# Optimization experiments

Hardware: AMD Instinct MI355X
Metric: run time of the kernel (lower is better)

## Reference

```python
import jax, jax.numpy as jnp
import numpy as np

B, D, E, K, C = 16384, 256, 16, 4, 10
EPS = 1e-5  # torch LayerNorm default eps


def setup_inputs() -> dict:
    key = jax.random.key(0)
    ks = jax.random.split(key, 5)
    s = 0.02
    return {
        "features": jax.random.normal(ks[0], (B, D), dtype=jnp.float32),
        "router_w": jax.random.normal(ks[1], (D, E), dtype=jnp.float32) * s,
        "router_b": jnp.zeros((E,), dtype=jnp.float32),
        "ln_g": jnp.ones((E, D), dtype=jnp.float32),
        "ln_b": jnp.zeros((E, D), dtype=jnp.float32),
        "w1": jax.random.normal(ks[2], (E, D, D), dtype=jnp.float32) * s,
        "b1": jnp.zeros((E, D), dtype=jnp.float32),
        "w2": jax.random.normal(ks[3], (E, D, C), dtype=jnp.float32) * s,
        "b2": jnp.zeros((E, C), dtype=jnp.float32),
    }


def reference(features, router_w, router_b, ln_g, ln_b, w1, b1, w2, b2):
    # Router: [B,D] @ [D,E] -> [B,E]
    gate_logits = features @ router_w + router_b
    gate_probs = jax.nn.softmax(gate_logits, axis=-1)
    topk_vals, topk_idx = jax.lax.top_k(gate_probs, K)  # [B,K]
    topk_vals = topk_vals / topk_vals.sum(axis=-1, keepdims=True)

    # Shared LayerNorm statistics (per-sample), per-expert affine.
    mu = features.mean(axis=-1, keepdims=True)
    var = ((features - mu) ** 2).mean(axis=-1, keepdims=True)
    xhat = (features - mu) * jax.lax.rsqrt(var + EPS)  # [B,D]
    xn = ln_g[:, None, :] * xhat[None, :, :] + ln_b[:, None, :]  # [E,B,D]

    # All experts densely (batched GEMMs), exact (erf) GELU like torch.
    h = jax.nn.gelu(jnp.einsum('ebd,edh->ebh', xn, w1) + b1[:, None, :],
                    approximate=False)  # [E,B,D]
    all_logits_e = jnp.einsum('ebh,ehc->ebc', h, w2) + b2[:, None, :]  # [E,B,C]
    all_logits = jnp.transpose(all_logits_e, (1, 0, 2))  # [B,E,C]

    # Gather top-k experts' logits and mix their softmaxed probs.
    idx = jnp.broadcast_to(topk_idx[:, :, None], (features.shape[0], K, C))
    selected = jnp.take_along_axis(all_logits, idx, axis=1)  # [B,K,C]
    market_probs = (topk_vals[:, :, None] * jax.nn.softmax(selected, axis=-1)).sum(axis=1)

    all_probs = jax.nn.softmax(all_logits_e, axis=-1)  # [E,B,C]
    return market_probs, all_probs, gate_probs
```

## Files before the change

kernel.cpp:

```cpp
#include <hip/hip_runtime.h>
#include <hip/hip_bf16.h>
#include <stdint.h>


typedef __bf16 bf16;
typedef __bf16 bf16x8 __attribute__((ext_vector_type(8)));
typedef __bf16 bf16x4 __attribute__((ext_vector_type(4)));
typedef float  f32x4  __attribute__((ext_vector_type(4)));

#define XK_OFF   0UL
#define W1T_OFF  8388608UL
#define W2T_OFF  10485760UL
#define B1P_OFF  10616832UL
#define TKI_OFF  10633216UL
#define TKW_OFF  10895360UL

#define APROBS_OFF 163840UL
#define GATE_OFF   2785280UL

#define LOG2E 1.4426950408889634f

__device__ __forceinline__ void gl_lds16(const void* g, void* l) {
  __builtin_amdgcn_global_load_lds((const __attribute__((address_space(1))) void*)g,
                                   (__attribute__((address_space(3))) void*)l, 16, 0, 0);
}

__device__ __forceinline__ uint32_t cvt_pk_bf16(float a, float b) {
  uint32_t r;
  asm("v_cvt_pk_bf16_f32 %0, %1, %2" : "=v"(r) : "v"(a), "v"(b));
  return r;
}

__device__ __forceinline__ float gelu_f(float x) {
  float e = __builtin_amdgcn_exp2f(-2.45541f * x);
  return x * __builtin_amdgcn_rcpf(e + 1.0f);
}

__global__ __launch_bounds__(256) void k_pre(const float* __restrict__ feat,
                                             const float* __restrict__ rw,
                                             const float* __restrict__ rb,
                                             const float* __restrict__ ln_g,
                                             const float* __restrict__ ln_b,
                                             const float* __restrict__ b1,
                                             const float* __restrict__ w1,
                                             const float* __restrict__ w2,
                                             float* __restrict__ out,
                                             char* __restrict__ ws) {
  __shared__ __align__(16) char sm[20736];
  const int bid = blockIdx.x;
  const int t = threadIdx.x;

  if (bid < 256) {
    float (*tile)[68] = (float(*)[68])sm;
    const int e = bid >> 4, kt = (bid >> 2) & 3, nt = bid & 3;
    {
      const int r = t >> 2, cs = t & 3;
      const float* src = w1 + ((size_t)e * 256 + kt * 64 + r) * 256 + nt * 64 + cs * 16;
#pragma unroll
      for (int j = 0; j < 4; ++j) {
        float4 v = *(const float4*)(src + j * 4);
        *(float4*)(&tile[r][cs * 16 + j * 4]) = v;
      }
    }
    __syncthreads();
    {
      const int rn = t >> 2, ks = t & 3;
      const int n = nt * 64 + rn;
      bf16* base = (bf16*)(ws + W1T_OFF) + (size_t)e * 65536;
      float pb = 0.f;
#pragma unroll
      for (int j = 0; j < 4; ++j) {
        int kc = ks * 16 + j * 4;
        int k0 = kt * 64 + kc;
        float4 g4 = *(const float4*)(ln_g + e * 256 + k0);
        float4 l4 = *(const float4*)(ln_b + e * 256 + k0);
        float t0 = tile[kc + 0][rn], t1 = tile[kc + 1][rn];
        float t2 = tile[kc + 2][rn], t3 = tile[kc + 3][rn];
        bf16x4 o;
        o[0] = (bf16)(t0 * g4.x);
        o[1] = (bf16)(t1 * g4.y);
        o[2] = (bf16)(t2 * g4.z);
        o[3] = (bf16)(t3 * g4.w);
        pb += l4.x * t0 + l4.y * t1 + l4.z * t2 + l4.w * t3;
        *(bf16x4*)(base + (k0 >> 5) * 8192 + n * 32 + (k0 & 31)) = o;
      }
      pb += __shfl_xor(pb, 1);
      pb += __shfl_xor(pb, 2);
      if (ks == 0) {
        if (kt == 0) pb += b1[e * 256 + n];
        atomicAdd((float*)(ws + B1P_OFF) + e * 256 + n, pb);
      }
    }
  } else if (bid < 272) {
    const int e = bid - 256;
    const int c = t >> 4, hs = t & 15;
    bf16* dst = (bf16*)(ws + W2T_OFF) + (size_t)e * 4096 + c * 256 + hs * 16;
#pragma unroll
    for (int j4 = 0; j4 < 4; ++j4) {
      bf16x4 o;
#pragma unroll
      for (int j = 0; j < 4; ++j) {
        int h = hs * 16 + j4 * 4 + j;
        float v = (c < 10) ? w2[((size_t)e * 256 + h) * 10 + c] : 0.0f;
        o[j] = (bf16)v;
      }
      *(bf16x4*)(dst + j4 * 4) = o;
    }
  } else {
    float (*rwt)[260] = (float(*)[260])sm;
    float (*xrow)[256] = (float(*)[256])(sm + 16640);
    const int w = t >> 6, l = t & 63;
    const int b = (bid - 272) * 4 + w;

    float4 x4 = *(const float4*)(feat + (size_t)b * 256 + l * 4);

#pragma unroll
    for (int i = 0; i < 16; ++i) {
      int idx = t + 256 * i;
      rwt[idx & 15][idx >> 4] = rw[idx];
    }
    *(float4*)(&xrow[w][l * 4]) = x4;

    float s = x4.x + x4.y + x4.z + x4.w;
    float s2 = x4.x * x4.x + x4.y * x4.y + x4.z * x4.z + x4.w * x4.w;
#pragma unroll
    for (int off = 1; off < 64; off <<= 1) {
      s += __shfl_xor(s, off);
      s2 += __shfl_xor(s2, off);
    }
    float mu = s * (1.0f / 256.0f);
    float var = s2 * (1.0f / 256.0f) - mu * mu;
    float rstd = __builtin_amdgcn_rsqf(var + 1e-5f);
    bf16x4 hb;
    hb[0] = (bf16)((x4.x - mu) * rstd);
    hb[1] = (bf16)((x4.y - mu) * rstd);
    hb[2] = (bf16)((x4.z - mu) * rstd);
    hb[3] = (bf16)((x4.w - mu) * rstd);
    *(bf16x4*)((bf16*)(ws + XK_OFF) + ((size_t)(b >> 7) * 32768) + (l >> 3) * 4096 +
               (b & 127) * 32 + (l & 7) * 4) = hb;

    __syncthreads();

    const int e = l & 15, q = l >> 4;
    float g = 0.f;
#pragma unroll
    for (int i = 0; i < 16; ++i) {
      float4 xv = *(const float4*)(&xrow[w][q * 64 + i * 4]);
      float4 wv = *(const float4*)(&rwt[e][q * 64 + i * 4]);
      g += xv.x * wv.x + xv.y * wv.y + xv.z * wv.z + xv.w * wv.w;
    }
    g += __shfl_xor(g, 16);
    g += __shfl_xor(g, 32);
    g += rb[e];

    float m = g;
#pragma unroll
    for (int off = 1; off < 16; off <<= 1) m = fmaxf(m, __shfl_xor(m, off));
    float p = __builtin_amdgcn_exp2f((g - m) * LOG2E);
    float sum = p;
#pragma unroll
    for (int off = 1; off < 16; off <<= 1) sum += __shfl_xor(sum, off);
    float prob = p * __builtin_amdgcn_rcpf(sum);
    if (q == 0) out[GATE_OFF + (size_t)b * 16 + e] = prob;

    float pv[16];
#pragma unroll
    for (int i = 0; i < 16; ++i) pv[i] = __shfl(prob, i);
    int idxk[4];
    float valk[4];
#pragma unroll
    for (int k = 0; k < 4; ++k) {
      float best = pv[0];
      int bi = 0;
#pragma unroll
      for (int i = 1; i < 16; ++i) {
        if (pv[i] > best) { best = pv[i]; bi = i; }
      }
      valk[k] = best;
      idxk[k] = bi;
#pragma unroll
      for (int i = 0; i < 16; ++i) pv[i] = (i == bi) ? -1.0f : pv[i];
    }
    float wsum = valk[0] + valk[1] + valk[2] + valk[3];
    float rn = __builtin_amdgcn_rcpf(wsum);
    if (l == 0) {
      int4 iv = {idxk[0], idxk[1], idxk[2], idxk[3]};
      float4 wv = {valk[0] * rn, valk[1] * rn, valk[2] * rn, valk[3] * rn};
      *(int4*)(ws + TKI_OFF + (size_t)b * 16) = iv;
      *(float4*)(ws + TKW_OFF + (size_t)b * 16) = wv;
    }
  }
}

__global__ __launch_bounds__(512, 4) void k_moe(const char* __restrict__ ws,
                                                const float* __restrict__ b2g,
                                                float* __restrict__ out) {
  __shared__ __align__(16) char smem[49152];
  const int lin = blockIdx.x;
  const int e = (lin >> 3) & 15;
  const int mt = (lin & 7) * 16 + (lin >> 7);
  const int m0 = mt * 128;
  const int t = threadIdx.x;
  const int wid = t >> 6, l = t & 63;
  const int lq = l >> 4, lr = l & 15;
  const int wnb = wid >> 1;
  const int wsb = wid & 1;

  const uint16_t* xk = (const uint16_t*)(ws + XK_OFF) + (size_t)mt * 32768;
  const uint16_t* w1km = (const uint16_t*)(ws + W1T_OFF) + (size_t)e * 65536;
  const uint16_t* w2t = (const uint16_t*)(ws + W2T_OFF) + (size_t)e * 4096;
  const float* b1p = (const float*)(ws + B1P_OFF) + e * 256;

  const int pn = t >> 3, hf = (t >> 2) & 1, sl = t & 3;
  const int srcoff = (2 * pn + hf) * 32 + ((sl ^ (pn & 3)) * 8);
  const uint16_t* sW = w1km + srcoff;
  const uint16_t* sX = xk + srcoff;

  gl_lds16(sW, smem + wid * 1024);
  gl_lds16(sW + 4096, smem + 8192 + wid * 1024);
  gl_lds16(sX, smem + 32768 + wid * 1024);

  const int pr = lr >> 1;
  const int fsw = (lr & 1) * 64 + ((lq ^ (pr & 3)) << 4);
  const int aoffb = (wnb * 32 + pr) * 128 + fsw;
  const int xoffb = (wsb * 32 + pr) * 128 + fsw;

  f32x4 zz = {0.f, 0.f, 0.f, 0.f};
  f32x4 acc[4][4];
#pragma unroll
  for (int mi = 0; mi < 4; ++mi)
#pragma unroll
    for (int nj = 0; nj < 4; ++nj) acc[mi][nj] = zz;

  __syncthreads();
#pragma unroll
  for (int kt = 0; kt < 8; ++kt) {
    const int buf = kt & 1;
    if (kt < 7) {
      const uint16_t* a = sW + (kt + 1) * 8192;
      char* dW = smem + (buf ^ 1) * 16384 + wid * 1024;
      gl_lds16(a, dW);
      gl_lds16(a + 4096, dW + 8192);
      gl_lds16(sX + (kt + 1) * 4096, smem + 32768 + (buf ^ 1) * 8192 + wid * 1024);
    }
    bf16x8 af[4], xf[4];
#pragma unroll
    for (int mi = 0; mi < 4; ++mi)
      af[mi] = *(const bf16x8*)(smem + buf * 16384 + aoffb + mi * 1024);
#pragma unroll
    for (int nj = 0; nj < 4; ++nj)
      xf[nj] = *(const bf16x8*)(smem + 32768 + buf * 8192 + xoffb + nj * 1024);
    __builtin_amdgcn_s_setprio(1);
#pragma unroll
    for (int mi = 0; mi < 4; ++mi)
#pragma unroll
      for (int nj = 0; nj < 4; ++nj)
        acc[mi][nj] = __builtin_amdgcn_mfma_f32_16x16x32_bf16(af[mi], xf[nj], acc[mi][nj], 0, 0, 0);
    __builtin_amdgcn_s_setprio(0);
    __syncthreads();
  }

  const uint16_t* w2l = w2t + lr * 256 + wnb * 64 + lq * 4;
  uint2 w2f[4];
#pragma unroll
  for (int mi = 0; mi < 4; ++mi)
    w2f[mi] = *(const uint2*)(w2l + mi * 16);
  uint4 ub0 = {w2f[0].x, w2f[0].y, w2f[1].x, w2f[1].y};
  uint4 ub1 = {w2f[2].x, w2f[2].y, w2f[3].x, w2f[3].y};

  float4 bn[4];
#pragma unroll
  for (int mi = 0; mi < 4; ++mi)
    bn[mi] = *(const float4*)(b1p + wnb * 64 + mi * 16 + lq * 4);

  f32x4 acc2[4];
#pragma unroll
  for (int nj = 0; nj < 4; ++nj) {
    uint32_t pk[8];
#pragma unroll
    for (int mi = 0; mi < 4; ++mi) {
      float g0 = gelu_f(acc[mi][nj][0] + bn[mi].x);
      float g1 = gelu_f(acc[mi][nj][1] + bn[mi].y);
      float g2 = gelu_f(acc[mi][nj][2] + bn[mi].z);
      float g3 = gelu_f(acc[mi][nj][3] + bn[mi].w);
      pk[mi * 2] = cvt_pk_bf16(g0, g1);
      pk[mi * 2 + 1] = cvt_pk_bf16(g2, g3);
    }
    uint4 ua0 = {pk[0], pk[1], pk[2], pk[3]};
    uint4 ua1 = {pk[4], pk[5], pk[6], pk[7]};
    f32x4 a2 = zz;
    a2 = __builtin_amdgcn_mfma_f32_16x16x32_bf16(__builtin_bit_cast(bf16x8, ua0),
                                                 __builtin_bit_cast(bf16x8, ub0), a2, 0, 0, 0);
    a2 = __builtin_amdgcn_mfma_f32_16x16x32_bf16(__builtin_bit_cast(bf16x8, ua1),
                                                 __builtin_bit_cast(bf16x8, ub1), a2, 0, 0, 0);
    acc2[nj] = a2;
  }

  const int pswz = (lq ^ ((lr >> 1) & 3)) << 4;
  {
    const int pbase = wnb * 1024 + lr * 64 + pswz;
#pragma unroll
    for (int nj = 0; nj < 4; ++nj)
      *(f32x4*)(smem + pbase + (wsb * 4 + nj) * 4096) = acc2[nj];
  }
  __syncthreads();

  {
    const int rbase = (wsb * 4 + wnb) * 4096 + lr * 64 + pswz;
    f32x4 r0 = *(const f32x4*)(smem + rbase);
    f32x4 r1 = *(const f32x4*)(smem + rbase + 1024);
    f32x4 r2 = *(const f32x4*)(smem + rbase + 2048);
    f32x4 r3 = *(const f32x4*)(smem + rbase + 3072);
    f32x4 tot;
#pragma unroll
    for (int j = 0; j < 4; ++j) tot[j] = (r0[j] + r1[j]) + (r2[j] + r3[j]);

    const int c = lr;
    float bias2 = (c < 10) ? b2g[e * 10 + c] : 0.0f;
#pragma unroll
    for (int rg = 0; rg < 4; ++rg) {
      float logit = tot[rg] + bias2;
      float ex = (c < 10) ? __builtin_amdgcn_exp2f(logit * LOG2E) : 0.0f;
      float sm = ex;
#pragma unroll
      for (int off = 1; off < 16; off <<= 1) sm += __shfl_xor(sm, off);
      if (c < 10) {
        float pr_ = ex * __builtin_amdgcn_rcpf(sm);
        size_t row = (size_t)e * 16384 + (m0 + wsb * 64 + wnb * 16 + lq * 4 + rg);
        out[APROBS_OFF + row * 10 + c] = pr_;
      }
    }
  }
}

__global__ __launch_bounds__(256) void k_market(const char* __restrict__ ws,
                                                float* __restrict__ out) {
  const int b = blockIdx.x * 256 + threadIdx.x;
  int4 id = *(const int4*)(ws + TKI_OFF + (size_t)b * 16);
  float4 wv = *(const float4*)(ws + TKW_OFF + (size_t)b * 16);
  const int ids[4] = {id.x, id.y, id.z, id.w};
  const float wss[4] = {wv.x, wv.y, wv.z, wv.w};
  float m[10];
#pragma unroll
  for (int c = 0; c < 10; ++c) m[c] = 0.f;
#pragma unroll
  for (int k = 0; k < 4; ++k) {
    const float* ap = out + APROBS_OFF + ((size_t)ids[k] * 16384 + b) * 10;
#pragma unroll
    for (int c = 0; c < 10; ++c) m[c] += wss[k] * ap[c];
  }
#pragma unroll
  for (int c = 0; c < 10; ++c) out[(size_t)b * 10 + c] = m[c];
}

extern "C" void kernel_launch(void* const* d_in, const int* in_sizes, int n_in,
                              void* d_out, int out_size, void* d_ws, size_t ws_size,
                              hipStream_t stream) {
  (void)in_sizes; (void)n_in; (void)out_size; (void)ws_size;
  const float* feat = (const float*)d_in[0];
  const float* rw   = (const float*)d_in[1];
  const float* rb   = (const float*)d_in[2];
  const float* ln_g = (const float*)d_in[3];
  const float* ln_b = (const float*)d_in[4];
  const float* w1   = (const float*)d_in[5];
  const float* b1   = (const float*)d_in[6];
  const float* w2   = (const float*)d_in[7];
  const float* b2   = (const float*)d_in[8];
  float* out = (float*)d_out;
  char* ws = (char*)d_ws;

  hipMemsetAsync(ws + B1P_OFF, 0, 16384, stream);
  hipLaunchKernelGGL(k_pre, dim3(4368), dim3(256), 0, stream,
                     feat, rw, rb, ln_g, ln_b, b1, w1, w2, out, ws);
  hipLaunchKernelGGL(k_moe, dim3(2048), dim3(512), 0, stream, ws, b2, out);
  hipLaunchKernelGGL(k_market, dim3(64), dim3(256), 0, stream, ws, out);
}
```

Measured before the change: 76.33 us.

## Fuse top-k market mixing into expert epilogue and drop atomic bias prep

The separate k_market kernel is removed. Each k_moe epilogue thread now reads its row's top-k indices and weights and atomically adds its weighted expert probability into the market output, which is zeroed by a memset up front. The w1 prep blocks now loop over all four k tiles inside one block, so the folded bias is written directly instead of accumulated with atomics, and the bias memset goes away. This saves a kernel launch and a re-read of all_probs, at the cost of about 655K float atomics, a non-deterministic summation order, and fewer, longer-running prep blocks.

Result: slower. 83.69 us (+9.6%).

```diff
diff --git a/kernel.cpp b/kernel.cpp
--- a/kernel.cpp
+++ b/kernel.cpp
@@ -50,49 +50,50 @@
   const int bid = blockIdx.x;
   const int t = threadIdx.x;
 
-  if (bid < 256) {
+  if (bid < 64) {
     float (*tile)[68] = (float(*)[68])sm;
-    const int e = bid >> 4, kt = (bid >> 2) & 3, nt = bid & 3;
-    {
-      const int r = t >> 2, cs = t & 3;
-      const float* src = w1 + ((size_t)e * 256 + kt * 64 + r) * 256 + nt * 64 + cs * 16;
-#pragma unroll
-      for (int j = 0; j < 4; ++j) {
-        float4 v = *(const float4*)(src + j * 4);
-        *(float4*)(&tile[r][cs * 16 + j * 4]) = v;
-      }
-    }
-    __syncthreads();
-    {
-      const int rn = t >> 2, ks = t & 3;
-      const int n = nt * 64 + rn;
-      bf16* base = (bf16*)(ws + W1T_OFF) + (size_t)e * 65536;
-      float pb = 0.f;
-#pragma unroll
-      for (int j = 0; j < 4; ++j) {
-        int kc = ks * 16 + j * 4;
-        int k0 = kt * 64 + kc;
-        float4 g4 = *(const float4*)(ln_g + e * 256 + k0);
-        float4 l4 = *(const float4*)(ln_b + e * 256 + k0);
-        float t0 = tile[kc + 0][rn], t1 = tile[kc + 1][rn];
-        float t2 = tile[kc + 2][rn], t3 = tile[kc + 3][rn];
-        bf16x4 o;
-        o[0] = (bf16)(t0 * g4.x);
-        o[1] = (bf16)(t1 * g4.y);
-        o[2] = (bf16)(t2 * g4.z);
-        o[3] = (bf16)(t3 * g4.w);
-        pb += l4.x * t0 + l4.y * t1 + l4.z * t2 + l4.w * t3;
-        *(bf16x4*)(base + (k0 >> 5) * 8192 + n * 32 + (k0 & 31)) = o;
-      }
-      pb += __shfl_xor(pb, 1);
-      pb += __shfl_xor(pb, 2);
-      if (ks == 0) {
-        if (kt == 0) pb += b1[e * 256 + n];
-        atomicAdd((float*)(ws + B1P_OFF) + e * 256 + n, pb);
-      }
-    }
-  } else if (bid < 272) {
-    const int e = bid - 256;
+    const int e = bid >> 2, nt = bid & 3;
+    const int rn = t >> 2, ks = t & 3;
+    const int n = nt * 64 + rn;
+    bf16* base = (bf16*)(ws + W1T_OFF) + (size_t)e * 65536;
+    float pb = 0.f;
+#pragma unroll
+    for (int kt = 0; kt < 4; ++kt) {
+      {
+        const float* src = w1 + ((size_t)e * 256 + kt * 64 + rn) * 256 + nt * 64 + ks * 16;
+#pragma unroll
+        for (int j = 0; j < 4; ++j) {
+          float4 v = *(const float4*)(src + j * 4);
+          *(float4*)(&tile[rn][ks * 16 + j * 4]) = v;
+        }
+      }
+      __syncthreads();
+      {
+#pragma unroll
+        for (int j = 0; j < 4; ++j) {
+          int kc = ks * 16 + j * 4;
+          int k0 = kt * 64 + kc;
+          float4 g4 = *(const float4*)(ln_g + e * 256 + k0);
+          float4 l4 = *(const float4*)(ln_b + e * 256 + k0);
+          float t0 = tile[kc + 0][rn], t1 = tile[kc + 1][rn];
+          float t2 = tile[kc + 2][rn], t3 = tile[kc + 3][rn];
+          bf16x4 o;
+          o[0] = (bf16)(t0 * g4.x);
+          o[1] = (bf16)(t1 * g4.y);
+          o[2] = (bf16)(t2 * g4.z);
+          o[3] = (bf16)(t3 * g4.w);
+          pb += l4.x * t0 + l4.y * t1 + l4.z * t2 + l4.w * t3;
+          *(bf16x4*)(base + (k0 >> 5) * 8192 + n * 32 + (k0 & 31)) = o;
+        }
+      }
+      __syncthreads();
+    }
+    pb += __shfl_xor(pb, 1);
+    pb += __shfl_xor(pb, 2);
+    if (ks == 0)
+      ((float*)(ws + B1P_OFF))[e * 256 + n] = pb + b1[e * 256 + n];
+  } else if (bid < 80) {
+    const int e = bid - 64;
     const int c = t >> 4, hs = t & 15;
     bf16* dst = (bf16*)(ws + W2T_OFF) + (size_t)e * 4096 + c * 256 + hs * 16;
 #pragma unroll
@@ -110,7 +111,7 @@
     float (*rwt)[260] = (float(*)[260])sm;
     float (*xrow)[256] = (float(*)[256])(sm + 16640);
     const int w = t >> 6, l = t & 63;
-    const int b = (bid - 272) * 4 + w;
+    const int b = (bid - 80) * 4 + w;
 
     float4 x4 = *(const float4*)(feat + (size_t)b * 256 + l * 4);
 
@@ -182,10 +183,10 @@
       for (int i = 0; i < 16; ++i) pv[i] = (i == bi) ? -1.0f : pv[i];
     }
     float wsum = valk[0] + valk[1] + valk[2] + valk[3];
-    float rn = __builtin_amdgcn_rcpf(wsum);
+    float rn2 = __builtin_amdgcn_rcpf(wsum);
     if (l == 0) {
       int4 iv = {idxk[0], idxk[1], idxk[2], idxk[3]};
-      float4 wv = {valk[0] * rn, valk[1] * rn, valk[2] * rn, valk[3] * rn};
+      float4 wv = {valk[0] * rn2, valk[1] * rn2, valk[2] * rn2, valk[3] * rn2};
       *(int4*)(ws + TKI_OFF + (size_t)b * 16) = iv;
       *(float4*)(ws + TKW_OFF + (size_t)b * 16) = wv;
     }
@@ -319,6 +320,7 @@
     float bias2 = (c < 10) ? b2g[e * 10 + c] : 0.0f;
 #pragma unroll
     for (int rg = 0; rg < 4; ++rg) {
+      const int b = m0 + wsb * 64 + wnb * 16 + lq * 4 + rg;
       float logit = tot[rg] + bias2;
       float ex = (c < 10) ? __builtin_amdgcn_exp2f(logit * LOG2E) : 0.0f;
       float sm = ex;
@@ -326,31 +328,15 @@
       for (int off = 1; off < 16; off <<= 1) sm += __shfl_xor(sm, off);
       if (c < 10) {
         float pr_ = ex * __builtin_amdgcn_rcpf(sm);
-        size_t row = (size_t)e * 16384 + (m0 + wsb * 64 + wnb * 16 + lq * 4 + rg);
-        out[APROBS_OFF + row * 10 + c] = pr_;
-      }
-    }
-  }
-}
-
-__global__ __launch_bounds__(256) void k_market(const char* __restrict__ ws,
-                                                float* __restrict__ out) {
-  const int b = blockIdx.x * 256 + threadIdx.x;
-  int4 id = *(const int4*)(ws + TKI_OFF + (size_t)b * 16);
-  float4 wv = *(const float4*)(ws + TKW_OFF + (size_t)b * 16);
-  const int ids[4] = {id.x, id.y, id.z, id.w};
-  const float wss[4] = {wv.x, wv.y, wv.z, wv.w};
-  float m[10];
-#pragma unroll
-  for (int c = 0; c < 10; ++c) m[c] = 0.f;
-#pragma unroll
-  for (int k = 0; k < 4; ++k) {
-    const float* ap = out + APROBS_OFF + ((size_t)ids[k] * 16384 + b) * 10;
-#pragma unroll
-    for (int c = 0; c < 10; ++c) m[c] += wss[k] * ap[c];
-  }
-#pragma unroll
-  for (int c = 0; c < 10; ++c) out[(size_t)b * 10 + c] = m[c];
+        out[APROBS_OFF + ((size_t)e * 16384 + b) * 10 + c] = pr_;
+        int4 id = *(const int4*)(ws + TKI_OFF + (size_t)b * 16);
+        float4 wv = *(const float4*)(ws + TKW_OFF + (size_t)b * 16);
+        float wk = (id.x == e) ? wv.x : (id.y == e) ? wv.y
+                 : (id.z == e) ? wv.z : (id.w == e) ? wv.w : 0.0f;
+        if (wk != 0.0f) atomicAdd(out + (size_t)b * 10 + c, wk * pr_);
+      }
+    }
+  }
 }
 
 extern "C" void kernel_launch(void* const* d_in, const int* in_sizes, int n_in,
@@ -369,9 +355,8 @@
   float* out = (float*)d_out;
   char* ws = (char*)d_ws;
 
-  hipMemsetAsync(ws + B1P_OFF, 0, 16384, stream);
-  hipLaunchKernelGGL(k_pre, dim3(4368), dim3(256), 0, stream,
+  hipMemsetAsync(out, 0, 163840 * 4, stream);
+  hipLaunchKernelGGL(k_pre, dim3(4176), dim3(256), 0, stream,
                      feat, rw, rb, ln_g, ln_b, b1, w1, w2, out, ws);
   hipLaunchKernelGGL(k_moe, dim3(2048), dim3(512), 0, stream, ws, b2, out);
-  hipLaunchKernelGGL(k_market, dim3(64), dim3(256), 0, stream, ws, out);
-}
+}
```
